# Kernel optimization log

Measured on AMD Instinct MI355X. Metric: run time of the kernel, lower is better.

Reference implementation:

```python
import jax, jax.numpy as jnp
import numpy as np

NC = 80          # num classes
NBINS = 16       # DFL bins = reg_max_bbox_loss + 1
REG_MAX = 15     # BboxLoss reg_max (m.reg_max - 1)
GAMMA = 1.5      # focal gamma (h['fl_gamma'])
ALPHA = 0.25     # focal alpha
BOX_W, CLS_W, DFL_W = 7.5, 0.5, 1.5
LEVELS = [(80, 80), (40, 40), (20, 20)]  # 640x640 image, strides 8/16/32


def make_anchor_points():
    pts = []
    for h, w in LEVELS:
        ys, xs = np.meshgrid(np.arange(h) + 0.5, np.arange(w) + 0.5, indexing='ij')
        pts.append(np.stack([xs.ravel(), ys.ravel()], -1))
    return jnp.asarray(np.concatenate(pts, 0), jnp.float32)  # (8400, 2)


def setup_inputs() -> dict:
    B, A = 32, 8400
    key = jax.random.key(0)
    k = jax.random.split(key, 6)
    anchor_points = make_anchor_points()
    pred_dist = jax.random.normal(k[0], (B, A, 4 * NBINS), jnp.float32)
    pred_scores = jax.random.normal(k[1], (B, A, NC), jnp.float32)
    fg_mask = jax.random.uniform(k[2], (B, A)) < 0.05
    # valid xyxy targets around each anchor -> ltrb in (0.5, 6) < REG_MAX - 0.01
    off1 = jax.random.uniform(k[3], (B, A, 2), minval=0.5, maxval=6.0)
    off2 = jax.random.uniform(k[4], (B, A, 2), minval=0.5, maxval=6.0)
    target_bboxes = jnp.concatenate([anchor_points - off1, anchor_points + off2], -1)
    target_scores = jax.random.uniform(k[5], (B, A, NC)) * fg_mask[..., None].astype(jnp.float32)
    return dict(pred_dist=pred_dist, pred_scores=pred_scores,
                anchor_points=anchor_points, target_bboxes=target_bboxes,
                target_scores=target_scores, fg_mask=fg_mask)


def _ciou(b1, b2, eps=1e-7):
    # xyxy CIoU, matches ultralytics bbox_iou(xywh=False, CIoU=True)
    b1x1, b1y1, b1x2, b1y2 = b1[..., 0], b1[..., 1], b1[..., 2], b1[..., 3]
    b2x1, b2y1, b2x2, b2y2 = b2[..., 0], b2[..., 1], b2[..., 2], b2[..., 3]
    w1, h1 = b1x2 - b1x1, b1y2 - b1y1 + eps
    w2, h2 = b2x2 - b2x1, b2y2 - b2y1 + eps
    inter = (jnp.minimum(b1x2, b2x2) - jnp.maximum(b1x1, b2x1)).clip(0) * \
            (jnp.minimum(b1y2, b2y2) - jnp.maximum(b1y1, b2y1)).clip(0)
    union = w1 * h1 + w2 * h2 - inter + eps
    iou = inter / union
    cw = jnp.maximum(b1x2, b2x2) - jnp.minimum(b1x1, b2x1)
    ch = jnp.maximum(b1y2, b2y2) - jnp.minimum(b1y1, b2y1)
    c2 = cw * cw + ch * ch + eps
    rho2 = ((b2x1 + b2x2 - b1x1 - b1x2) ** 2 + (b2y1 + b2y2 - b1y1 - b1y2) ** 2) / 4.0
    v = (4.0 / (jnp.pi ** 2)) * (jnp.arctan(w2 / h2) - jnp.arctan(w1 / h1)) ** 2
    alpha = jax.lax.stop_gradient(v / (v - iou + (1.0 + eps)))  # torch.no_grad()
    return iou - (rho2 / c2 + v * alpha)


def _loss_core(pred_dist, pred_scores, anchor_points, target_bboxes, target_scores, fg_mask):
    B, A, _ = pred_scores.shape
    dt = pred_scores.dtype
    tss = jnp.maximum(target_scores.sum(), 1.0)  # target_scores_sum

    # ---- focal BCE (pos_weight=1) ----
    p = jax.nn.sigmoid(pred_scores)
    bce = target_scores * jax.nn.softplus(-pred_scores) + (1.0 - target_scores) * jax.nn.softplus(pred_scores)
    p_t = target_scores * p + (1.0 - target_scores) * (1.0 - p)
    alpha_f = target_scores * ALPHA + (1.0 - target_scores) * (1.0 - ALPHA)
    loss_cls = (bce * alpha_f * (1.0 - p_t) ** GAMMA).sum() / tss

    # ---- bbox decode (DFL expectation) ----
    proj = jnp.arange(NBINS, dtype=dt)
    logits = pred_dist.reshape(B, A, 4, NBINS)
    dist = jax.nn.softmax(logits, axis=-1) @ proj                     # (B,A,4) ltrb
    pred_bboxes = jnp.concatenate([anchor_points - dist[..., :2],
                                   anchor_points + dist[..., 2:]], -1)

    fg = fg_mask.astype(dt)
    bbox_weight = target_scores.sum(-1) * fg                          # masked weight (B,A)

    # ---- CIoU loss (mask replaces masked_select) ----
    iou = _ciou(pred_bboxes, target_bboxes)
    loss_iou = ((1.0 - iou) * bbox_weight).sum() / tss

    # ---- DFL loss: left/right weighted cross-entropy ----
    target_ltrb = jnp.clip(jnp.concatenate([anchor_points - target_bboxes[..., :2],
                                            target_bboxes[..., 2:] - anchor_points], -1),
                           0.0, REG_MAX - 0.01)                       # (B,A,4)
    tl = jnp.floor(target_ltrb).astype(jnp.int32)
    tr = tl + 1
    wl = tr.astype(dt) - target_ltrb
    wr = 1.0 - wl
    logp = jax.nn.log_softmax(logits, axis=-1)                        # (B,A,4,NBINS)
    ce_l = -jnp.take_along_axis(logp, tl[..., None], axis=-1)[..., 0]
    ce_r = -jnp.take_along_axis(logp, tr[..., None], axis=-1)[..., 0]
    loss_dfl = (((ce_l * wl + ce_r * wr).mean(-1)) * bbox_weight).sum() / tss

    return jnp.stack([BOX_W * loss_iou, CLS_W * loss_cls, DFL_W * loss_dfl])


def reference(pred_dist, pred_scores, anchor_points, target_bboxes, target_scores, fg_mask):
    loss = _loss_core(pred_dist, pred_scores, anchor_points, target_bboxes, target_scores, fg_mask)
    return loss  # weighted [box, cls, dfl]; total = loss.sum()
```

## Files before the change

### kernel.cpp

```cpp
#include <hip/hip_runtime.h>
#include <math.h>

#define NC      80
#define A_TOT   8400
#define B_TOT   32
#define BA      (B_TOT * A_TOT)
#define NGRP    (BA / 16)
#define NCHUNK  (BA / 64)
#define BLOCK   256
#define NB_TARGET 3150

__device__ __forceinline__ float wave_sum(float v) {
    #pragma unroll
    for (int off = 32; off > 0; off >>= 1) v += __shfl_down(v, off, 64);
    return v;
}

__global__ __launch_bounds__(BLOCK) void loss_main(
    const float* __restrict__ pred_dist,
    const float* __restrict__ pred_scores,
    const float* __restrict__ anchor_points,
    const float* __restrict__ target_bboxes,
    const float* __restrict__ target_scores,
    const int* __restrict__ fgmask,
    float* __restrict__ partials,
    int nb, int fgb)
{
    __shared__ float red[4][4];

    const int tid  = threadIdx.x;
    const int lane = tid & 63;
    const int wid  = tid >> 6;

    const float4* ps4 = (const float4*)pred_scores;
    const float4* ts4 = (const float4*)target_scores;
    const float4* tb4 = (const float4*)target_bboxes;

    float cls_acc = 0.0f, iou_acc = 0.0f, dfl_acc = 0.0f, ts_acc = 0.0f;

    if ((int)blockIdx.x < fgb) {
        const int fstride = fgb * 4;
        for (int c = blockIdx.x * 4 + wid; c < NCHUNK; c += fstride) {
            const long abase = (long)c * 64;
            const int myfg = fgmask[abase + lane];
            unsigned long long m = __ballot(myfg != 0);

            long gc = -1; float xc = 0.0f;
            float4 tbc = make_float4(0,0,0,0), tsc = make_float4(0,0,0,0);
            if (m) {
                int b = __ffsll((long long)m) - 1; m &= m - 1;
                gc = abase + b;
                xc  = pred_dist[gc * 64 + lane];
                tbc = tb4[gc];
                tsc = (lane < 20) ? ts4[gc * 20 + lane] : make_float4(0,0,0,0);
            }
            while (gc >= 0) {
                long gn = -1; float xn = 0.0f;
                float4 tbn = make_float4(0,0,0,0), tsn = make_float4(0,0,0,0);
                if (m) {
                    int b = __ffsll((long long)m) - 1; m &= m - 1;
                    gn = abase + b;
                    xn  = pred_dist[gn * 64 + lane];
                    tbn = tb4[gn];
                    tsn = (lane < 20) ? ts4[gn * 20 + lane] : make_float4(0,0,0,0);
                }

                float w = tsc.x + tsc.y + tsc.z + tsc.w;
                #pragma unroll
                for (int off = 1; off < 64; off <<= 1) w += __shfl_xor(w, off, 64);

                const int a = (int)(gc % A_TOT);
                const float ax = anchor_points[2 * a];
                const float ay = anchor_points[2 * a + 1];
                const int side = lane >> 4;
                const int k    = lane & 15;
                const float x  = xc;

                float tval = (side == 0) ? ax - tbc.x :
                             (side == 1) ? ay - tbc.y :
                             (side == 2) ? tbc.z - ax : tbc.w - ay;
                float tcl = fminf(fmaxf(tval, 0.0f), 14.99f);
                int   tl  = (int)tcl;
                float wl  = (float)(tl + 1) - tcl;
                float wr  = 1.0f - wl;

                float mx = x;
                mx = fmaxf(mx, __shfl_xor(mx, 1));
                mx = fmaxf(mx, __shfl_xor(mx, 2));
                mx = fmaxf(mx, __shfl_xor(mx, 4));
                mx = fmaxf(mx, __shfl_xor(mx, 8));

                float ex = __expf(x - mx);
                float se = ex;
                float nu = (float)k * ex;
                float ls = ((k == tl) ? wl : (k == tl + 1) ? wr : 0.0f) * x;
                #pragma unroll
                for (int off = 1; off < 16; off <<= 1) {
                    se += __shfl_xor(se, off);
                    nu += __shfl_xor(nu, off);
                    ls += __shfl_xor(ls, off);
                }
                float dist = nu * __builtin_amdgcn_rcpf(se);
                float ce   = mx + __logf(se) - ls;

                float d0 = __shfl(dist, 0),  d1 = __shfl(dist, 16);
                float d2 = __shfl(dist, 32), d3 = __shfl(dist, 48);
                float c0 = __shfl(ce, 0),    c1 = __shfl(ce, 16);
                float c2 = __shfl(ce, 32),   c3 = __shfl(ce, 48);

                if (lane == 0) {
                    dfl_acc += 0.25f * (c0 + c1 + c2 + c3) * w;

                    const float eps = 1e-7f;
                    float px1 = ax - d0, py1 = ay - d1;
                    float px2 = ax + d2, py2 = ay + d3;
                    float w1 = px2 - px1, h1 = py2 - py1 + eps;
                    float w2 = tbc.z - tbc.x, h2 = tbc.w - tbc.y + eps;
                    float iw = fmaxf(fminf(px2, tbc.z) - fmaxf(px1, tbc.x), 0.0f);
                    float ih = fmaxf(fminf(py2, tbc.w) - fmaxf(py1, tbc.y), 0.0f);
                    float inter = iw * ih;
                    float uni = w1 * h1 + w2 * h2 - inter + eps;
                    float iou = inter / uni;
                    float cw = fmaxf(px2, tbc.z) - fminf(px1, tbc.x);
                    float ch = fmaxf(py2, tbc.w) - fminf(py1, tbc.y);
                    float c2d = cw * cw + ch * ch + eps;
                    float dx = tbc.x + tbc.z - px1 - px2;
                    float dy = tbc.y + tbc.w - py1 - py2;
                    float rho2 = (dx * dx + dy * dy) * 0.25f;
                    const float c4pi2 = 0.40528473456935109f;
                    float dat = atanf(w2 / h2) - atanf(w1 / h1);
                    float v = c4pi2 * dat * dat;
                    float alpha = v / (v - iou + (1.0f + eps));
                    float ciou = iou - (rho2 / c2d + v * alpha);
                    iou_acc += (1.0f - ciou) * w;
                }

                gc = gn; xc = xn; tbc = tbn; tsc = tsn;
            }
        }
    } else {
        const int q   = lane & 3;
        const int alg = lane >> 2;
        const int dstride = (nb - fgb) * 4;
        for (int grp = (blockIdx.x - fgb) * 4 + wid; grp < NGRP; grp += dstride) {
            const long g0   = (long)grp * 16;
            const long base = (g0 + alg) * 20 + q;

            const int fgm = fgmask[g0 + alg];

            float4 tvl[5];
            #pragma unroll
            for (int j = 0; j < 5; ++j) tvl[j] = make_float4(0.f, 0.f, 0.f, 0.f);
            if (fgm) {
                #pragma unroll
                for (int j = 0; j < 5; ++j) tvl[j] = ts4[base + 4 * j];
            }

            #pragma unroll
            for (int j = 0; j < 5; ++j) {
                float4 pv = ps4[base + 4 * j];
                float px[4] = {pv.x, pv.y, pv.z, pv.w};
                float tx[4] = {tvl[j].x, tvl[j].y, tvl[j].z, tvl[j].w};
                #pragma unroll
                for (int cc = 0; cc < 4; ++cc) {
                    float xx = px[cc];
                    float tv = tx[cc];
                    float e   = __expf(-fabsf(xx));
                    float ope = 1.0f + e;
                    float lp  = __logf(ope);
                    float sp  = fmaxf(xx, 0.0f) + lp;
                    float bce = sp - tv * xx;
                    float pp  = __builtin_amdgcn_rcpf(ope);
                    float p   = (xx >= 0.0f) ? pp : (1.0f - pp);
                    float u   = fmaf(p, 1.0f - 2.0f * tv, tv);
                    u = fmaxf(u, 0.0f);
                    float af  = 0.75f - 0.5f * tv;
                    float su  = __builtin_amdgcn_sqrtf(u);
                    cls_acc += bce * af * (u * su);
                    ts_acc  += tv;
                }
            }
        }
    }

    float v0 = wave_sum(iou_acc);
    float v1 = wave_sum(cls_acc);
    float v2 = wave_sum(ts_acc);
    float v3 = wave_sum(dfl_acc);
    if (lane == 0) { red[0][wid] = v0; red[1][wid] = v1; red[2][wid] = v2; red[3][wid] = v3; }
    __syncthreads();
    if (tid == 0) {
        float r0 = 0, r1 = 0, r2 = 0, r3 = 0;
        #pragma unroll
        for (int i = 0; i < 4; ++i) { r0 += red[0][i]; r1 += red[1][i]; r2 += red[2][i]; r3 += red[3][i]; }
        partials[0 * nb + blockIdx.x] = r0;
        partials[1 * nb + blockIdx.x] = r1;
        partials[2 * nb + blockIdx.x] = r2;
        partials[3 * nb + blockIdx.x] = r3;
    }
}

__global__ __launch_bounds__(BLOCK) void loss_reduce(
    const float* __restrict__ partials, int nb, float* __restrict__ out)
{
    __shared__ float red[4][4];
    int tid = threadIdx.x;
    float s0 = 0, s1 = 0, s2 = 0, s3 = 0;
    for (int i = tid; i < nb; i += BLOCK) {
        s0 += partials[i];
        s1 += partials[nb + i];
        s2 += partials[2 * nb + i];
        s3 += partials[3 * nb + i];
    }
    s0 = wave_sum(s0); s1 = wave_sum(s1); s2 = wave_sum(s2); s3 = wave_sum(s3);
    int wid = tid >> 6;
    if ((tid & 63) == 0) { red[0][wid] = s0; red[1][wid] = s1; red[2][wid] = s2; red[3][wid] = s3; }
    __syncthreads();
    if (tid == 0) {
        float r0 = 0, r1 = 0, r2 = 0, r3 = 0;
        #pragma unroll
        for (int i = 0; i < 4; ++i) { r0 += red[0][i]; r1 += red[1][i]; r2 += red[2][i]; r3 += red[3][i]; }
        float tss = fmaxf(r2, 1.0f);
        out[0] = 7.5f * r0 / tss;
        out[1] = 0.5f * r1 / tss;
        out[2] = 1.5f * r3 / tss;
    }
}

extern "C" void kernel_launch(void* const* d_in, const int* in_sizes, int n_in,
                              void* d_out, int out_size, void* d_ws, size_t ws_size,
                              hipStream_t stream) {
    const float* pred_dist     = (const float*)d_in[0];
    const float* pred_scores   = (const float*)d_in[1];
    const float* anchor_points = (const float*)d_in[2];
    const float* target_bboxes = (const float*)d_in[3];
    const float* target_scores = (const float*)d_in[4];
    const int*   fgmask        = (const int*)d_in[5];

    int nb = (int)(ws_size / (4 * sizeof(float)));
    if (nb > NB_TARGET) nb = NB_TARGET;
    if (nb < 2) nb = 2;
    int fgb = nb / 3;
    if (fgb < 1) fgb = 1;

    float* partials = (float*)d_ws;
    loss_main<<<nb, BLOCK, 0, stream>>>(
        pred_dist, pred_scores, anchor_points, target_bboxes, target_scores,
        fgmask, partials, nb, fgb);
    loss_reduce<<<1, BLOCK, 0, stream>>>(partials, nb, (float*)d_out);
}
```

Baseline: 216.1 us.

## Software-pipeline class-loss loop with register prefetch and shrink grid

Restructures the dense class-loss loop into a software-pipelined form. Each wave now issues the next group's pred_scores loads (and its fg mask read) before computing the current group, and fetches target_scores afterwards, hiding global memory latency behind the transcendental math. It also lowers the block count target and gives a smaller share of blocks to the foreground/DFL path, so each block runs more iterations. The cost is higher register pressure from the double-buffered float4 arrays, plus a redundant load on the final iteration.

New measurement: 221.1 us. +2.3%, slower.

```diff
diff --git a/kernel.cpp b/kernel.cpp
--- a/kernel.cpp
+++ b/kernel.cpp
@@ -8,7 +8,7 @@
 #define NGRP    (BA / 16)
 #define NCHUNK  (BA / 64)
 #define BLOCK   256
-#define NB_TARGET 3150
+#define NB_TARGET 1400
 
 __device__ __forceinline__ float wave_sum(float v) {
     #pragma unroll
@@ -141,44 +141,71 @@
     } else {
         const int q   = lane & 3;
         const int alg = lane >> 2;
-        const int dstride = (nb - fgb) * 4;
-        for (int grp = (blockIdx.x - fgb) * 4 + wid; grp < NGRP; grp += dstride) {
-            const long g0   = (long)grp * 16;
-            const long base = (g0 + alg) * 20 + q;
-
-            const int fgm = fgmask[g0 + alg];
-
-            float4 tvl[5];
+        const int dwaves = (nb - fgb) * 4;
+        long grp = (long)(blockIdx.x - fgb) * 4 + wid;
+
+        if (grp < NGRP) {
+            long g0   = grp * 16;
+            long base = (g0 + alg) * 20 + q;
+            int fgm_c = fgmask[g0 + alg];
+            float4 pc[5], tc[5];
             #pragma unroll
-            for (int j = 0; j < 5; ++j) tvl[j] = make_float4(0.f, 0.f, 0.f, 0.f);
-            if (fgm) {
-                #pragma unroll
-                for (int j = 0; j < 5; ++j) tvl[j] = ts4[base + 4 * j];
-            }
-
+            for (int j = 0; j < 5; ++j) pc[j] = ps4[base + 4 * j];
             #pragma unroll
-            for (int j = 0; j < 5; ++j) {
-                float4 pv = ps4[base + 4 * j];
-                float px[4] = {pv.x, pv.y, pv.z, pv.w};
-                float tx[4] = {tvl[j].x, tvl[j].y, tvl[j].z, tvl[j].w};
-                #pragma unroll
-                for (int cc = 0; cc < 4; ++cc) {
-                    float xx = px[cc];
-                    float tv = tx[cc];
-                    float e   = __expf(-fabsf(xx));
-                    float ope = 1.0f + e;
-                    float lp  = __logf(ope);
-                    float sp  = fmaxf(xx, 0.0f) + lp;
-                    float bce = sp - tv * xx;
-                    float pp  = __builtin_amdgcn_rcpf(ope);
-                    float p   = (xx >= 0.0f) ? pp : (1.0f - pp);
-                    float u   = fmaf(p, 1.0f - 2.0f * tv, tv);
-                    u = fmaxf(u, 0.0f);
-                    float af  = 0.75f - 0.5f * tv;
-                    float su  = __builtin_amdgcn_sqrtf(u);
-                    cls_acc += bce * af * (u * su);
-                    ts_acc  += tv;
-                }
+            for (int j = 0; j < 5; ++j) tc[j] = make_float4(0.f, 0.f, 0.f, 0.f);
+            if (fgm_c) {
+                #pragma unroll
+                for (int j = 0; j < 5; ++j) tc[j] = ts4[base + 4 * j];
+            }
+
+            while (true) {
+                long nxt   = grp + dwaves;
+                bool has_n = (nxt < NGRP);
+                long gsafe = has_n ? nxt : grp;
+                long gn0   = gsafe * 16;
+                long basen = (gn0 + alg) * 20 + q;
+                int  fgm_n = fgmask[gn0 + alg];
+                float4 pn[5];
+                #pragma unroll
+                for (int j = 0; j < 5; ++j) pn[j] = ps4[basen + 4 * j];
+
+                #pragma unroll
+                for (int j = 0; j < 5; ++j) {
+                    float px[4] = {pc[j].x, pc[j].y, pc[j].z, pc[j].w};
+                    float tx[4] = {tc[j].x, tc[j].y, tc[j].z, tc[j].w};
+                    #pragma unroll
+                    for (int cc = 0; cc < 4; ++cc) {
+                        float xx = px[cc];
+                        float tv = tx[cc];
+                        float e   = __expf(-fabsf(xx));
+                        float ope = 1.0f + e;
+                        float lp  = __logf(ope);
+                        float sp  = fmaxf(xx, 0.0f) + lp;
+                        float bce = sp - tv * xx;
+                        float pp  = __builtin_amdgcn_rcpf(ope);
+                        float p   = (xx >= 0.0f) ? pp : (1.0f - pp);
+                        float u   = fmaf(p, 1.0f - 2.0f * tv, tv);
+                        u = fmaxf(u, 0.0f);
+                        float af  = 0.75f - 0.5f * tv;
+                        float su  = __builtin_amdgcn_sqrtf(u);
+                        cls_acc += bce * af * (u * su);
+                        ts_acc  += tv;
+                    }
+                }
+
+                float4 tn[5];
+                #pragma unroll
+                for (int j = 0; j < 5; ++j) tn[j] = make_float4(0.f, 0.f, 0.f, 0.f);
+                if (fgm_n && has_n) {
+                    #pragma unroll
+                    for (int j = 0; j < 5; ++j) tn[j] = ts4[basen + 4 * j];
+                }
+
+                if (!has_n) break;
+                grp = nxt;
+                fgm_c = fgm_n;
+                #pragma unroll
+                for (int j = 0; j < 5; ++j) { pc[j] = pn[j]; tc[j] = tn[j]; }
             }
         }
     }
@@ -240,7 +267,7 @@
     int nb = (int)(ws_size / (4 * sizeof(float)));
     if (nb > NB_TARGET) nb = NB_TARGET;
     if (nb < 2) nb = 2;
-    int fgb = nb / 3;
+    int fgb = nb / 4;
     if (fgb < 1) fgb = 1;
 
     float* partials = (float*)d_ws;
```
